# Performance work log

Measured on AMD Instinct MI355X. Metric: run time of the kernel, lower is better.

Reference implementation:

```python
import jax, jax.numpy as jnp
import numpy as np
import math

D_MODEL, D_HEAD = 1024, 64
N_HEADS = D_MODEL // D_HEAD  # 16
EPS = 1e-6

def rms_norm(x, scale, eps=EPS):
    ms = jnp.mean(x * x, axis=-1, keepdims=True)
    return x * scale * jax.lax.rsqrt(ms + eps)

def apply_rotary_emb(x, theta):
    # theta: (..., d) rotates first 2*d dims of x
    d = theta.shape[-1]
    x1, x2, x3 = x[..., :d], x[..., d:2 * d], x[..., 2 * d:]
    cos, sin = jnp.cos(theta), jnp.sin(theta)
    return jnp.concatenate([x1 * cos - x2 * sin, x2 * cos + x1 * sin, x3], axis=-1)

def make_freqs():
    d4 = D_HEAD // 4  # 16
    log_min, log_max = math.log(math.pi), math.log(10.0 * math.pi)
    f = np.exp(np.linspace(log_min, log_max, N_HEADS * d4 + 1, dtype=np.float64)[:-1])
    return jnp.asarray(f.reshape(d4, N_HEADS).T, dtype=jnp.float32)  # (n_heads, d_head//4)

def setup_inputs() -> dict:
    key = jax.random.key(0)
    ks = jax.random.split(key, 8)
    n, l = 4, 1024
    x = jax.random.normal(ks[0], (n, l, D_MODEL), jnp.float32)
    pos = jax.random.uniform(ks[1], (n, l, 2), jnp.float32)
    attn_mask = jnp.ones((1, 1, l, l), dtype=bool)
    cond = jax.random.normal(ks[2], (n, 1, D_MODEL), jnp.float32)
    norm_w = jax.random.normal(ks[3], (D_MODEL, D_MODEL), jnp.float32) * 0.02
    qkv_w = jax.random.normal(ks[4], (3 * D_MODEL, D_MODEL), jnp.float32) * (D_MODEL ** -0.5)
    qk_scale = jnp.ones((N_HEADS, 1, 1), jnp.float32)
    out_w = jax.random.normal(ks[5], (D_MODEL, D_MODEL), jnp.float32) * 0.02
    freqs = make_freqs()
    return {"x": x, "pos": pos, "attn_mask": attn_mask, "cond": cond,
            "norm_w": norm_w, "qkv_w": qkv_w, "qk_scale": qk_scale,
            "freqs": freqs, "out_w": out_w}

def reference(x, pos, attn_mask, cond, norm_w, qkv_w, qk_scale, freqs, out_w):
    n, l, d = x.shape
    # AdaRMSNorm
    h = rms_norm(x, jnp.einsum('nlc,dc->nld', cond, norm_w) + 1.0)
    # QKV projection -> (n, h, l, e)
    qkv = jnp.einsum('nld,ed->nle', h, qkv_w)
    q, k, v = jnp.split(qkv, 3, axis=-1)
    split_heads = lambda t: t.reshape(n, l, N_HEADS, D_HEAD).transpose(0, 2, 1, 3)
    q, k, v = split_heads(q), split_heads(k), split_heads(v)
    # per-head RMSNorm (scale shape (h,1,1))
    q = rms_norm(q, qk_scale)
    k = rms_norm(k, qk_scale)
    # axial RoPE: theta (n, h, l, d_head//2)
    theta = jnp.concatenate([
        pos[:, None, :, 0:1] * freqs[None, :, None, :],
        pos[:, None, :, 1:2] * freqs[None, :, None, :],
    ], axis=-1)
    q = apply_rotary_emb(q, theta)
    k = apply_rotary_emb(k, theta)
    # SDPA
    scores = jnp.einsum('nhqe,nhke->nhqk', q, k) * (D_HEAD ** -0.5)
    scores = jnp.where(attn_mask, scores, jnp.float32(-1e30))
    attn = jax.nn.softmax(scores, axis=-1)
    o = jnp.einsum('nhqk,nhke->nhqe', attn, v)
    o = o.transpose(0, 2, 1, 3).reshape(n, l, d)
    return jnp.einsum('nld,ed->nle', o, out_w)
```

## Files before the change

### kernel.cpp

```cpp
#include <hip/hip_runtime.h>

typedef short bf16x8 __attribute__((ext_vector_type(8)));
typedef float f32x4 __attribute__((ext_vector_type(4)));

__device__ __forceinline__ float bf2f(ushort u) {
  union { unsigned int i; float f; } x; x.i = ((unsigned int)u) << 16; return x.f;
}
__device__ __forceinline__ ushort f2bf(float f) {
  union { float f; unsigned int i; } x; x.f = f;
  unsigned int r = x.i + 0x7fff + ((x.i >> 16) & 1);
  return (ushort)(r >> 16);
}
__device__ __forceinline__ unsigned int cvtpk_bf16(float a, float b) {
  unsigned int r;
  asm("v_cvt_pk_bf16_f32 %0, %1, %2" : "=v"(r) : "v"(a), "v"(b));
  return r;
}

__device__ __forceinline__ f32x4 mfma16(bf16x8 a, bf16x8 b, f32x4 c) {
  return __builtin_amdgcn_mfma_f32_16x16x32_bf16(a, b, c, 0, 0, 0);
}

__device__ __forceinline__ void gload_lds16(const void* g, void* l) {
  __builtin_amdgcn_global_load_lds(
      (const __attribute__((address_space(1))) void*)g,
      (__attribute__((address_space(3))) void*)l, 16, 0, 0);
}

__global__ __launch_bounds__(256) void f2bf_vec2(const float* __restrict__ a,
                                                 ushort* __restrict__ oa, int n4a,
                                                 const float* __restrict__ b,
                                                 ushort* __restrict__ ob, int n4b) {
  int i = blockIdx.x * 256 + threadIdx.x;
  const float* src;
  ushort* dst;
  int j;
  if (i < n4a) {
    src = a; dst = oa; j = i;
  } else {
    j = i - n4a;
    if (j >= n4b) return;
    src = b; dst = ob;
  }
  float4 v = ((const float4*)src)[j];
  ushort4 o;
  o.x = f2bf(v.x); o.y = f2bf(v.y); o.z = f2bf(v.z); o.w = f2bf(v.w);
  ((ushort4*)dst)[j] = o;
}

__global__ __launch_bounds__(256) void cond_gemv(const float* __restrict__ cond,
                                                 const float* __restrict__ nw,
                                                 float* __restrict__ sout) {
  const int w = threadIdx.x >> 6, lane = threadIdx.x & 63;
  const int idx = blockIdx.x * 4 + w;
  const int n_ = idx >> 10, d = idx & 1023;
  const float* cr = cond + n_ * 1024;
  const float* wr_ = nw + (size_t)d * 1024;
  float sum = 0.f;
#pragma unroll
  for (int c = lane; c < 1024; c += 64) sum += cr[c] * wr_[c];
#pragma unroll
  for (int off = 1; off < 64; off <<= 1) sum += __shfl_xor(sum, off);
  if (lane == 0) sout[idx] = sum + 1.0f;
}

__global__ __launch_bounds__(256) void rmsnorm_x(const float* __restrict__ x,
                                                 const float* __restrict__ s,
                                                 ushort* __restrict__ h, int L) {
  const int row = blockIdx.x;
  const int n_ = row / L;
  const int tid = threadIdx.x;
  __shared__ float red[4];
  float4 xv = ((const float4*)(x + (size_t)row * 1024))[tid];
  float ss = xv.x * xv.x + xv.y * xv.y + xv.z * xv.z + xv.w * xv.w;
#pragma unroll
  for (int off = 1; off < 64; off <<= 1) ss += __shfl_xor(ss, off);
  if ((tid & 63) == 0) red[tid >> 6] = ss;
  __syncthreads();
  float tot = red[0] + red[1] + red[2] + red[3];
  float r = rsqrtf(tot * (1.f / 1024.f) + 1e-6f);
  float4 sv = ((const float4*)(s + (size_t)n_ * 1024))[tid];
  ushort4 o;
  o.x = f2bf(xv.x * sv.x * r);
  o.y = f2bf(xv.y * sv.y * r);
  o.z = f2bf(xv.z * sv.z * r);
  o.w = f2bf(xv.w * sv.w * r);
  ((ushort4*)(h + (size_t)row * 1024))[tid] = o;
}

template <typename OT>
__global__ __launch_bounds__(256) void gemm_bt(const ushort* __restrict__ A,
                                               const ushort* __restrict__ B,
                                               OT* __restrict__ C, int M, int N,
                                               int K, int nbx) {
  __shared__ ushort As[2][128 * 32];
  __shared__ ushort Bs[2][128 * 32];
  const int tid = threadIdx.x;
  const int w = tid >> 6;
  const int lane = tid & 63;
  const int wr = w >> 1, wc = w & 1;
  const int lm = lane & 15, g = lane >> 4;
  const int qchunk = gridDim.x >> 3;
  const int swz = (blockIdx.x & 7) * qchunk + (blockIdx.x >> 3);
  const int bn = (swz % nbx) * 128;
  const int bm = (swz / nbx) * 128;
  f32x4 acc[4][4] = {};
  const int u_ = lane >> 3;
  const int pp = (lane & 7) ^ u_;
  const int srow = (u_ << 1) | (pp >> 2);
  const int scol = (pp & 3) * 8;
  const int rb = (lm >> 1) * 64 + (((((lm & 1) << 2) | g) ^ (lm >> 1)) << 3);

  auto stage = [&](int kt, int b) {
#pragma unroll
    for (int i = 0; i < 2; ++i) {
      const int c = w * 2 + i;
      gload_lds16(&A[(size_t)(bm + c * 16 + srow) * K + kt + scol],
                  &As[b][c * 512]);
      gload_lds16(&B[(size_t)(bn + c * 16 + srow) * K + kt + scol],
                  &Bs[b][c * 512]);
    }
  };

  const int NTK = K >> 5;
  stage(0, 0);
  stage(32, 1);
  for (int t = 0; t < NTK; ++t) {
    const int b = t & 1;
    if (t + 1 < NTK)
      asm volatile("s_waitcnt vmcnt(4)" ::: "memory");
    else
      asm volatile("s_waitcnt vmcnt(0)" ::: "memory");
    __builtin_amdgcn_s_barrier();
    bf16x8 af[4], bfr[4];
#pragma unroll
    for (int mi = 0; mi < 4; ++mi)
      af[mi] = *(const bf16x8*)&As[b][(wr * 4 + mi) * 512 + rb];
#pragma unroll
    for (int ni = 0; ni < 4; ++ni)
      bfr[ni] = *(const bf16x8*)&Bs[b][(wc * 4 + ni) * 512 + rb];
    asm volatile("s_waitcnt lgkmcnt(0)" ::: "memory");
    __builtin_amdgcn_sched_barrier(0);
    __builtin_amdgcn_s_barrier();
    if (t + 2 < NTK) stage((t + 2) << 5, b);
#pragma unroll
    for (int mi = 0; mi < 4; ++mi)
#pragma unroll
      for (int ni = 0; ni < 4; ++ni)
        acc[mi][ni] = mfma16(af[mi], bfr[ni], acc[mi][ni]);
  }
#pragma unroll
  for (int mi = 0; mi < 4; ++mi)
#pragma unroll
    for (int ni = 0; ni < 4; ++ni) {
      int col = bn + wc * 64 + ni * 16 + lm;
#pragma unroll
      for (int r = 0; r < 4; ++r) {
        int row = bm + wr * 64 + mi * 16 + g * 4 + r;
        float v = acc[mi][ni][r];
        if constexpr (sizeof(OT) == 2)
          C[(size_t)row * N + col] = (OT)f2bf(v);
        else
          C[(size_t)row * N + col] = (OT)v;
      }
    }
}

__global__ __launch_bounds__(256) void qkv_prep(
    const ushort* __restrict__ qkv, const float* __restrict__ pos,
    const float* __restrict__ qscale, const float* __restrict__ freqs,
    ushort* __restrict__ Qr, ushort* __restrict__ Kr, ushort* __restrict__ Vr,
    int L) {
  const int row = blockIdx.x;
  const int n_ = row / L;
  const int l = row - n_ * L;
  const int w = threadIdx.x >> 6, lane = threadIdx.x & 63;
  const float p0 = pos[row * 2 + 0], p1 = pos[row * 2 + 1];
  const int tl = lane & 31;
#pragma unroll
  for (int hi = 0; hi < 4; ++hi) {
    const int h = w * 4 + hi;
    const size_t ib = (size_t)row * 3072 + h * 64 + lane;
    float qv = bf2f(qkv[ib]);
    float kv = bf2f(qkv[ib + 1024]);
    float vv = bf2f(qkv[ib + 2048]);
    float sq = qv * qv, sk = kv * kv;
#pragma unroll
    for (int off = 1; off < 64; off <<= 1) {
      sq += __shfl_xor(sq, off);
      sk += __shfl_xor(sk, off);
    }
    const float sc = qscale[h];
    float qn = qv * sc * rsqrtf(sq * (1.f / 64.f) + 1e-6f);
    float kn = kv * sc * rsqrtf(sk * (1.f / 64.f) + 1e-6f);
    float th = ((tl < 16) ? p0 : p1) * freqs[h * 16 + (tl & 15)];
    float s_, c_;
    sincosf(th, &s_, &c_);
    float qo = __shfl_xor(qn, 32);
    float ko = __shfl_xor(kn, 32);
    float qr = (lane < 32) ? (qn * c_ - qo * s_) : (qn * c_ + qo * s_);
    float kr = (lane < 32) ? (kn * c_ - ko * s_) : (kn * c_ + ko * s_);
    const size_t ob = ((size_t)(n_ * 16 + h) * L + l) * 64 + lane;
    Qr[ob] = f2bf(qr * 0.18033688f);
    Kr[ob] = f2bf(kr);
    Vr[ob] = f2bf(vv);
  }
}

__global__ __launch_bounds__(256) void vtrans(const ushort* __restrict__ v,
                                              ushort* __restrict__ vt) {
  __shared__ ushort T[64][72];
  const int tid = threadIdx.x;
  const int nh = blockIdx.y;
  const int l0 = blockIdx.x * 64;
  const int lr = tid >> 2;
  const int d0 = (tid & 3) * 16;
  const ushort* src = v + ((size_t)nh * 1024 + l0 + lr) * 64 + d0;
  *(uint4*)&T[lr][d0] = *(const uint4*)src;
  *(uint4*)&T[lr][d0 + 8] = *(const uint4*)(src + 8);
  __syncthreads();
  const int d = tid >> 2;
  const int lc = (tid & 3) * 16;
  ushort tmp[16];
#pragma unroll
  for (int j = 0; j < 16; ++j) tmp[j] = T[lc + j][d];
  ushort* dst = vt + ((size_t)nh * 64 + d) * 1024 + l0 + lc;
  *(uint4*)dst = *(uint4*)&tmp[0];
  *(uint4*)(dst + 8) = *(uint4*)&tmp[8];
}

__global__ __launch_bounds__(256) void attn_kernel(
    const ushort* __restrict__ Q, const ushort* __restrict__ Kg,
    const ushort* __restrict__ Vtg, ushort* __restrict__ O, int L) {
  __shared__ ushort Ks[2][64 * 64];
  __shared__ ushort Vs[2][64 * 64];
  __shared__ ushort Pb[4][32 * 64];
  const int tid = threadIdx.x;
  const int w = tid >> 6, lane = tid & 63;
  const int lm = lane & 15, g = lane >> 4;
  const int swz = (blockIdx.x & 7) * 64 + (blockIdx.x >> 3);
  const int nh = swz >> 3;
  const int qt = swz & 7;
  const ushort* q = Q + (size_t)nh * L * 64;
  const ushort* k = Kg + (size_t)nh * L * 64;
  const ushort* vt = Vtg + (size_t)nh * 64 * L;
  const int qbase = qt * 128 + w * 32;
  bf16x8 qf[2][2];
#pragma unroll
  for (int qs = 0; qs < 2; ++qs)
#pragma unroll
    for (int kc = 0; kc < 2; ++kc)
      qf[qs][kc] = *(const bf16x8*)&q[(size_t)(qbase + qs * 16 + lm) * 64 +
                                      kc * 32 + g * 8];
  f32x4 ot[2][4] = {};
  f32x4 lsacc[2] = {};
  bf16x8 ones;
#pragma unroll
  for (int i = 0; i < 8; ++i) ones[i] = (short)0x3F80;
  const int sr = lane >> 3;
  const int ss = (lane & 7) ^ sr;

  auto stage = [&](int tt, int b) {
#pragma unroll
    for (int i = 0; i < 2; ++i) {
      const int r = w * 16 + i * 8 + sr;
      gload_lds16(&k[(size_t)(tt * 64 + r) * 64 + ss * 8],
                  &Ks[b][(w * 16 + i * 8) * 64]);
    }
#pragma unroll
    for (int i = 0; i < 2; ++i) {
      const int r = w * 16 + i * 8 + sr;
      gload_lds16(&vt[(size_t)r * L + tt * 64 + ss * 8],
                  &Vs[b][(w * 16 + i * 8) * 64]);
    }
  };

  stage(0, 0);
  __syncthreads();
  const int NT = L >> 6;
  for (int t = 0; t < NT; ++t) {
    const int cur = t & 1;
    if (t + 1 < NT) stage(t + 1, cur ^ 1);
    const ushort* ksb = &Ks[cur][0];
    f32x4 st[2][4] = {};
    __builtin_amdgcn_s_setprio(1);
#pragma unroll
    for (int t16 = 0; t16 < 4; ++t16) {
      const int r = t16 * 16 + lm;
#pragma unroll
      for (int kc = 0; kc < 2; ++kc) {
        bf16x8 a = *(const bf16x8*)&ksb[r * 64 + (((kc * 4 + g) ^ (lm & 7)) << 3)];
        st[0][t16] = mfma16(a, qf[0][kc], st[0][t16]);
        st[1][t16] = mfma16(a, qf[1][kc], st[1][t16]);
      }
    }
    __builtin_amdgcn_s_setprio(0);
    float e[2][4][4];
#pragma unroll
    for (int qs = 0; qs < 2; ++qs)
#pragma unroll
      for (int t16 = 0; t16 < 4; ++t16)
#pragma unroll
        for (int r = 0; r < 4; ++r)
          e[qs][t16][r] = __builtin_amdgcn_exp2f(st[qs][t16][r]);
    ushort* pb = &Pb[w][0];
#pragma unroll
    for (int qs = 0; qs < 2; ++qs)
#pragma unroll
      for (int t16 = 0; t16 < 4; ++t16) {
        unsigned int lo = cvtpk_bf16(e[qs][t16][0], e[qs][t16][1]);
        unsigned int hi = cvtpk_bf16(e[qs][t16][2], e[qs][t16][3]);
        const int slot = (t16 * 2 + (g >> 1)) ^ (lm & 7);
        *(uint2*)&pb[(qs * 16 + lm) * 64 + slot * 8 + (g & 1) * 4] =
            make_uint2(lo, hi);
      }
    asm volatile("s_waitcnt lgkmcnt(0)" ::: "memory");
    __builtin_amdgcn_sched_barrier(0);
    bf16x8 pf[2][2];
#pragma unroll
    for (int qs = 0; qs < 2; ++qs)
#pragma unroll
      for (int c = 0; c < 2; ++c)
        pf[qs][c] = *(const bf16x8*)&pb[(qs * 16 + lm) * 64 +
                                        (((c * 4 + g) ^ (lm & 7)) << 3)];
    const ushort* vsb = &Vs[cur][0];
    __builtin_amdgcn_s_setprio(1);
#pragma unroll
    for (int db = 0; db < 4; ++db) {
      const int d = db * 16 + lm;
#pragma unroll
      for (int c = 0; c < 2; ++c) {
        bf16x8 a = *(const bf16x8*)&vsb[d * 64 + (((c * 4 + g) ^ (lm & 7)) << 3)];
        ot[0][db] = mfma16(a, pf[0][c], ot[0][db]);
        ot[1][db] = mfma16(a, pf[1][c], ot[1][db]);
      }
    }
#pragma unroll
    for (int qs = 0; qs < 2; ++qs)
#pragma unroll
      for (int c = 0; c < 2; ++c)
        lsacc[qs] = mfma16(ones, pf[qs][c], lsacc[qs]);
    __builtin_amdgcn_s_setprio(0);
    __syncthreads();
  }
  const int n_ = nh >> 4, h = nh & 15;
#pragma unroll
  for (int qs = 0; qs < 2; ++qs) {
    const float inv = 1.f / lsacc[qs][0];
#pragma unroll
    for (int db = 0; db < 4; ++db) {
      unsigned int lo = cvtpk_bf16(ot[qs][db][0] * inv, ot[qs][db][1] * inv);
      unsigned int hi = cvtpk_bf16(ot[qs][db][2] * inv, ot[qs][db][3] * inv);
      size_t off = ((size_t)(n_ * L + qbase + qs * 16 + lm) * 1024) + h * 64 +
                   db * 16 + g * 4;
      *(uint2*)&O[off] = make_uint2(lo, hi);
    }
  }
}

extern "C" void kernel_launch(void* const* d_in, const int* in_sizes, int n_in,
                              void* d_out, int out_size, void* d_ws,
                              size_t ws_size, hipStream_t stream) {
  const float* x = (const float*)d_in[0];
  const float* pos = (const float*)d_in[1];
  const float* cond = (const float*)d_in[3];
  const float* norm_w = (const float*)d_in[4];
  const float* qkv_w = (const float*)d_in[5];
  const float* qk_scale = (const float*)d_in[6];
  const float* freqs = (const float*)d_in[7];
  const float* out_w = (const float*)d_in[8];
  float* out = (float*)d_out;
  const int L = 1024;

  char* wsb = (char*)d_ws;
  ushort* qkvw_bf = (ushort*)(wsb);
  ushort* outw_bf = (ushort*)(wsb + 6291456);
  float* s_cond = (float*)(wsb + 8388608);
  ushort* h_buf = (ushort*)(wsb + 8404992);
  ushort* qkv_buf = (ushort*)(wsb + 16793600);
  ushort* q_r = (ushort*)(wsb + 41959424);
  ushort* k_r = (ushort*)(wsb + 50348032);
  ushort* v_r = (ushort*)(wsb + 58736640);
  ushort* o_buf = (ushort*)(wsb + 67125248);
  ushort* vt_buf = h_buf;

  hipLaunchKernelGGL(f2bf_vec2, dim3(4096), dim3(256), 0, stream, qkv_w,
                     qkvw_bf, 786432, out_w, outw_bf, 262144);
  hipLaunchKernelGGL(cond_gemv, dim3(1024), dim3(256), 0, stream, cond, norm_w,
                     s_cond);
  hipLaunchKernelGGL(rmsnorm_x, dim3(4096), dim3(256), 0, stream, x, s_cond,
                     h_buf, L);
  hipLaunchKernelGGL(gemm_bt<ushort>, dim3(768), dim3(256), 0, stream, h_buf,
                     qkvw_bf, qkv_buf, 4096, 3072, 1024, 24);
  hipLaunchKernelGGL(qkv_prep, dim3(4096), dim3(256), 0, stream, qkv_buf, pos,
                     qk_scale, freqs, q_r, k_r, v_r, L);
  hipLaunchKernelGGL(vtrans, dim3(16, 64), dim3(256), 0, stream, v_r, vt_buf);
  hipLaunchKernelGGL(attn_kernel, dim3(512), dim3(256), 0, stream, q_r, k_r,
                     vt_buf, o_buf, L);
  hipLaunchKernelGGL(gemm_bt<float>, dim3(256), dim3(256), 0, stream, o_buf,
                     outw_bf, out, 4096, 1024, 1024, 8);
}
```

Baseline: 120.9 us.

## Switch attention to 32x32x16 MFMA and keep P in registers via permlane swap

```diff
diff --git a/kernel.cpp b/kernel.cpp
--- a/kernel.cpp
+++ b/kernel.cpp
@@ -2,6 +2,7 @@
 
 typedef short bf16x8 __attribute__((ext_vector_type(8)));
 typedef float f32x4 __attribute__((ext_vector_type(4)));
+typedef float f32x16 __attribute__((ext_vector_type(16)));
 
 __device__ __forceinline__ float bf2f(ushort u) {
   union { unsigned int i; float f; } x; x.i = ((unsigned int)u) << 16; return x.f;
@@ -19,6 +20,12 @@
 
 __device__ __forceinline__ f32x4 mfma16(bf16x8 a, bf16x8 b, f32x4 c) {
   return __builtin_amdgcn_mfma_f32_16x16x32_bf16(a, b, c, 0, 0, 0);
+}
+__device__ __forceinline__ f32x16 mfma32(bf16x8 a, bf16x8 b, f32x16 c) {
+  return __builtin_amdgcn_mfma_f32_32x32x16_bf16(a, b, c, 0, 0, 0);
+}
+__device__ __forceinline__ void plswap(unsigned int& a, unsigned int& b) {
+  asm volatile("v_permlane32_swap_b32 %0, %1" : "+v"(a), "+v"(b));
 }
 
 __device__ __forceinline__ void gload_lds16(const void* g, void* l) {
@@ -234,10 +241,9 @@
     const ushort* __restrict__ Vtg, ushort* __restrict__ O, int L) {
   __shared__ ushort Ks[2][64 * 64];
   __shared__ ushort Vs[2][64 * 64];
-  __shared__ ushort Pb[4][32 * 64];
   const int tid = threadIdx.x;
   const int w = tid >> 6, lane = tid & 63;
-  const int lm = lane & 15, g = lane >> 4;
+  const int l31 = lane & 31, h32 = lane >> 5;
   const int swz = (blockIdx.x & 7) * 64 + (blockIdx.x >> 3);
   const int nh = swz >> 3;
   const int qt = swz & 7;
@@ -245,15 +251,11 @@
   const ushort* k = Kg + (size_t)nh * L * 64;
   const ushort* vt = Vtg + (size_t)nh * 64 * L;
   const int qbase = qt * 128 + w * 32;
-  bf16x8 qf[2][2];
-#pragma unroll
-  for (int qs = 0; qs < 2; ++qs)
-#pragma unroll
-    for (int kc = 0; kc < 2; ++kc)
-      qf[qs][kc] = *(const bf16x8*)&q[(size_t)(qbase + qs * 16 + lm) * 64 +
-                                      kc * 32 + g * 8];
-  f32x4 ot[2][4] = {};
-  f32x4 lsacc[2] = {};
+  bf16x8 qf[4];
+#pragma unroll
+  for (int kt = 0; kt < 4; ++kt)
+    qf[kt] = *(const bf16x8*)&q[(size_t)(qbase + l31) * 64 + kt * 16 + h32 * 8];
+  f32x16 ot0 = {}, ot1 = {}, lsacc = {};
   bf16x8 ones;
 #pragma unroll
   for (int i = 0; i < 8; ++i) ones[i] = (short)0x3F80;
@@ -282,78 +284,63 @@
     const int cur = t & 1;
     if (t + 1 < NT) stage(t + 1, cur ^ 1);
     const ushort* ksb = &Ks[cur][0];
-    f32x4 st[2][4] = {};
+    f32x16 st0 = {}, st1 = {};
     __builtin_amdgcn_s_setprio(1);
 #pragma unroll
-    for (int t16 = 0; t16 < 4; ++t16) {
-      const int r = t16 * 16 + lm;
-#pragma unroll
-      for (int kc = 0; kc < 2; ++kc) {
-        bf16x8 a = *(const bf16x8*)&ksb[r * 64 + (((kc * 4 + g) ^ (lm & 7)) << 3)];
-        st[0][t16] = mfma16(a, qf[0][kc], st[0][t16]);
-        st[1][t16] = mfma16(a, qf[1][kc], st[1][t16]);
-      }
+    for (int kk = 0; kk < 4; ++kk) {
+      const int sl = (((kk * 2 + h32) ^ (l31 & 7)) << 3);
+      bf16x8 a0 = *(const bf16x8*)&ksb[l31 * 64 + sl];
+      bf16x8 a1 = *(const bf16x8*)&ksb[(32 + l31) * 64 + sl];
+      st0 = mfma32(a0, qf[kk], st0);
+      st1 = mfma32(a1, qf[kk], st1);
     }
     __builtin_amdgcn_s_setprio(0);
-    float e[2][4][4];
-#pragma unroll
-    for (int qs = 0; qs < 2; ++qs)
-#pragma unroll
-      for (int t16 = 0; t16 < 4; ++t16)
-#pragma unroll
-        for (int r = 0; r < 4; ++r)
-          e[qs][t16][r] = __builtin_amdgcn_exp2f(st[qs][t16][r]);
-    ushort* pb = &Pb[w][0];
-#pragma unroll
-    for (int qs = 0; qs < 2; ++qs)
-#pragma unroll
-      for (int t16 = 0; t16 < 4; ++t16) {
-        unsigned int lo = cvtpk_bf16(e[qs][t16][0], e[qs][t16][1]);
-        unsigned int hi = cvtpk_bf16(e[qs][t16][2], e[qs][t16][3]);
-        const int slot = (t16 * 2 + (g >> 1)) ^ (lm & 7);
-        *(uint2*)&pb[(qs * 16 + lm) * 64 + slot * 8 + (g & 1) * 4] =
-            make_uint2(lo, hi);
-      }
-    asm volatile("s_waitcnt lgkmcnt(0)" ::: "memory");
-    __builtin_amdgcn_sched_barrier(0);
-    bf16x8 pf[2][2];
-#pragma unroll
-    for (int qs = 0; qs < 2; ++qs)
-#pragma unroll
-      for (int c = 0; c < 2; ++c)
-        pf[qs][c] = *(const bf16x8*)&pb[(qs * 16 + lm) * 64 +
-                                        (((c * 4 + g) ^ (lm & 7)) << 3)];
+    bf16x8 pfm[4];
+#pragma unroll
+    for (int kt2 = 0; kt2 < 2; ++kt2) {
+      float e[16];
+#pragma unroll
+      for (int r = 0; r < 16; ++r)
+        e[r] = __builtin_amdgcn_exp2f(kt2 ? st1[r] : st0[r]);
+      unsigned int A0 = cvtpk_bf16(e[0], e[1]), A1 = cvtpk_bf16(e[2], e[3]);
+      unsigned int B0 = cvtpk_bf16(e[4], e[5]), B1 = cvtpk_bf16(e[6], e[7]);
+      unsigned int C0 = cvtpk_bf16(e[8], e[9]), C1 = cvtpk_bf16(e[10], e[11]);
+      unsigned int D0 = cvtpk_bf16(e[12], e[13]), D1 = cvtpk_bf16(e[14], e[15]);
+      plswap(A0, B0);
+      plswap(A1, B1);
+      plswap(C0, D0);
+      plswap(C1, D1);
+      union { unsigned int u[4]; bf16x8 v; } f0, f1;
+      f0.u[0] = A0; f0.u[1] = A1; f0.u[2] = B0; f0.u[3] = B1;
+      f1.u[0] = C0; f1.u[1] = C1; f1.u[2] = D0; f1.u[3] = D1;
+      pfm[kt2 * 2 + 0] = f0.v;
+      pfm[kt2 * 2 + 1] = f1.v;
+    }
     const ushort* vsb = &Vs[cur][0];
     __builtin_amdgcn_s_setprio(1);
 #pragma unroll
-    for (int db = 0; db < 4; ++db) {
-      const int d = db * 16 + lm;
-#pragma unroll
-      for (int c = 0; c < 2; ++c) {
-        bf16x8 a = *(const bf16x8*)&vsb[d * 64 + (((c * 4 + g) ^ (lm & 7)) << 3)];
-        ot[0][db] = mfma16(a, pf[0][c], ot[0][db]);
-        ot[1][db] = mfma16(a, pf[1][c], ot[1][db]);
-      }
-    }
-#pragma unroll
-    for (int qs = 0; qs < 2; ++qs)
-#pragma unroll
-      for (int c = 0; c < 2; ++c)
-        lsacc[qs] = mfma16(ones, pf[qs][c], lsacc[qs]);
+    for (int m = 0; m < 4; ++m) {
+      const int sl = (((m * 2 + h32) ^ (l31 & 7)) << 3);
+      bf16x8 a0 = *(const bf16x8*)&vsb[l31 * 64 + sl];
+      bf16x8 a1 = *(const bf16x8*)&vsb[(32 + l31) * 64 + sl];
+      ot0 = mfma32(a0, pfm[m], ot0);
+      ot1 = mfma32(a1, pfm[m], ot1);
+      lsacc = mfma32(ones, pfm[m], lsacc);
+    }
     __builtin_amdgcn_s_setprio(0);
     __syncthreads();
   }
+  const float inv = 1.f / lsacc[0];
   const int n_ = nh >> 4, h = nh & 15;
-#pragma unroll
-  for (int qs = 0; qs < 2; ++qs) {
-    const float inv = 1.f / lsacc[qs][0];
-#pragma unroll
-    for (int db = 0; db < 4; ++db) {
-      unsigned int lo = cvtpk_bf16(ot[qs][db][0] * inv, ot[qs][db][1] * inv);
-      unsigned int hi = cvtpk_bf16(ot[qs][db][2] * inv, ot[qs][db][3] * inv);
-      size_t off = ((size_t)(n_ * L + qbase + qs * 16 + lm) * 1024) + h * 64 +
-                   db * 16 + g * 4;
-      *(uint2*)&O[off] = make_uint2(lo, hi);
+  const size_t rowoff = ((size_t)(n_ * L + qbase + l31)) * 1024 + h * 64;
+#pragma unroll
+  for (int dt = 0; dt < 2; ++dt) {
+    const f32x16& o = dt ? ot1 : ot0;
+#pragma unroll
+    for (int qd = 0; qd < 4; ++qd) {
+      unsigned int w0 = cvtpk_bf16(o[qd * 4 + 0] * inv, o[qd * 4 + 1] * inv);
+      unsigned int w1 = cvtpk_bf16(o[qd * 4 + 2] * inv, o[qd * 4 + 3] * inv);
+      *(uint2*)&O[rowoff + dt * 32 + qd * 8 + h32 * 4] = make_uint2(w0, w1);
     }
   }
 }
```

Measured after the change: 124.8 us. 3.2% more time.

## Fuse weight cast with cond GEMV, and V transpose into QKV prep

Applied to the files above, without the earlier changes.

```diff
diff --git a/kernel.cpp b/kernel.cpp
--- a/kernel.cpp
+++ b/kernel.cpp
@@ -27,32 +27,29 @@
       (__attribute__((address_space(3))) void*)l, 16, 0, 0);
 }
 
-__global__ __launch_bounds__(256) void f2bf_vec2(const float* __restrict__ a,
-                                                 ushort* __restrict__ oa, int n4a,
-                                                 const float* __restrict__ b,
-                                                 ushort* __restrict__ ob, int n4b) {
-  int i = blockIdx.x * 256 + threadIdx.x;
-  const float* src;
-  ushort* dst;
-  int j;
-  if (i < n4a) {
-    src = a; dst = oa; j = i;
-  } else {
-    j = i - n4a;
-    if (j >= n4b) return;
-    src = b; dst = ob;
-  }
-  float4 v = ((const float4*)src)[j];
-  ushort4 o;
-  o.x = f2bf(v.x); o.y = f2bf(v.y); o.z = f2bf(v.z); o.w = f2bf(v.w);
-  ((ushort4*)dst)[j] = o;
-}
-
-__global__ __launch_bounds__(256) void cond_gemv(const float* __restrict__ cond,
-                                                 const float* __restrict__ nw,
-                                                 float* __restrict__ sout) {
+__global__ __launch_bounds__(256) void prep0(
+    const float* __restrict__ qkv_w, ushort* __restrict__ qkvw_bf,
+    const float* __restrict__ out_w, ushort* __restrict__ outw_bf,
+    const float* __restrict__ cond, const float* __restrict__ nw,
+    float* __restrict__ sout) {
+  const int b = blockIdx.x;
+  if (b < 4096) {
+    const float* src;
+    ushort* dst;
+    int j;
+    if (b < 3072) {
+      src = qkv_w; dst = qkvw_bf; j = b * 256 + threadIdx.x;
+    } else {
+      src = out_w; dst = outw_bf; j = (b - 3072) * 256 + threadIdx.x;
+    }
+    float4 v = ((const float4*)src)[j];
+    ushort4 o;
+    o.x = f2bf(v.x); o.y = f2bf(v.y); o.z = f2bf(v.z); o.w = f2bf(v.w);
+    ((ushort4*)dst)[j] = o;
+    return;
+  }
   const int w = threadIdx.x >> 6, lane = threadIdx.x & 63;
-  const int idx = blockIdx.x * 4 + w;
+  const int idx = (b - 4096) * 4 + w;
   const int n_ = idx >> 10, d = idx & 1023;
   const float* cr = cond + n_ * 1024;
   const float* wr_ = nw + (size_t)d * 1024;
@@ -166,20 +163,26 @@
     }
 }
 
-__global__ __launch_bounds__(256) void qkv_prep(
+__global__ __launch_bounds__(256) void qkv_prep_t(
     const ushort* __restrict__ qkv, const float* __restrict__ pos,
     const float* __restrict__ qscale, const float* __restrict__ freqs,
-    ushort* __restrict__ Qr, ushort* __restrict__ Kr, ushort* __restrict__ Vr,
+    ushort* __restrict__ Qr, ushort* __restrict__ Kr, ushort* __restrict__ Vt,
     int L) {
-  const int row = blockIdx.x;
-  const int n_ = row / L;
-  const int l = row - n_ * L;
-  const int w = threadIdx.x >> 6, lane = threadIdx.x & 63;
-  const float p0 = pos[row * 2 + 0], p1 = pos[row * 2 + 1];
+  __shared__ ushort T[64][72];
+  const int tid = threadIdx.x;
+  const int w = tid >> 6, lane = tid & 63;
+  const int bid = blockIdx.x;
+  const int nh = bid >> 4;
+  const int lc = bid & 15;
+  const int n_ = nh >> 4, h = nh & 15;
+  const int l0 = lc * 64;
+  const float sc = qscale[h];
   const int tl = lane & 31;
-#pragma unroll
-  for (int hi = 0; hi < 4; ++hi) {
-    const int h = w * 4 + hi;
+  const float fr = freqs[h * 16 + (tl & 15)];
+#pragma unroll
+  for (int i = 0; i < 16; ++i) {
+    const int r = i * 4 + w;
+    const int row = n_ * L + l0 + r;
     const size_t ib = (size_t)row * 3072 + h * 64 + lane;
     float qv = bf2f(qkv[ib]);
     float kv = bf2f(qkv[ib + 1024]);
@@ -190,41 +193,28 @@
       sq += __shfl_xor(sq, off);
       sk += __shfl_xor(sk, off);
     }
-    const float sc = qscale[h];
     float qn = qv * sc * rsqrtf(sq * (1.f / 64.f) + 1e-6f);
     float kn = kv * sc * rsqrtf(sk * (1.f / 64.f) + 1e-6f);
-    float th = ((tl < 16) ? p0 : p1) * freqs[h * 16 + (tl & 15)];
+    const float p0 = pos[row * 2 + 0], p1 = pos[row * 2 + 1];
+    float th = ((tl < 16) ? p0 : p1) * fr;
     float s_, c_;
     sincosf(th, &s_, &c_);
     float qo = __shfl_xor(qn, 32);
     float ko = __shfl_xor(kn, 32);
     float qr = (lane < 32) ? (qn * c_ - qo * s_) : (qn * c_ + qo * s_);
     float kr = (lane < 32) ? (kn * c_ - ko * s_) : (kn * c_ + ko * s_);
-    const size_t ob = ((size_t)(n_ * 16 + h) * L + l) * 64 + lane;
+    const size_t ob = ((size_t)nh * L + l0 + r) * 64 + lane;
     Qr[ob] = f2bf(qr * 0.18033688f);
     Kr[ob] = f2bf(kr);
-    Vr[ob] = f2bf(vv);
-  }
-}
-
-__global__ __launch_bounds__(256) void vtrans(const ushort* __restrict__ v,
-                                              ushort* __restrict__ vt) {
-  __shared__ ushort T[64][72];
-  const int tid = threadIdx.x;
-  const int nh = blockIdx.y;
-  const int l0 = blockIdx.x * 64;
-  const int lr = tid >> 2;
-  const int d0 = (tid & 3) * 16;
-  const ushort* src = v + ((size_t)nh * 1024 + l0 + lr) * 64 + d0;
-  *(uint4*)&T[lr][d0] = *(const uint4*)src;
-  *(uint4*)&T[lr][d0 + 8] = *(const uint4*)(src + 8);
+    T[r][lane] = f2bf(vv);
+  }
   __syncthreads();
   const int d = tid >> 2;
-  const int lc = (tid & 3) * 16;
+  const int lc4 = (tid & 3) * 16;
   ushort tmp[16];
 #pragma unroll
-  for (int j = 0; j < 16; ++j) tmp[j] = T[lc + j][d];
-  ushort* dst = vt + ((size_t)nh * 64 + d) * 1024 + l0 + lc;
+  for (int j = 0; j < 16; ++j) tmp[j] = T[lc4 + j][d];
+  ushort* dst = Vt + ((size_t)nh * 64 + d) * L + l0 + lc4;
   *(uint4*)dst = *(uint4*)&tmp[0];
   *(uint4*)(dst + 8) = *(uint4*)&tmp[8];
 }
@@ -380,21 +370,17 @@
   ushort* qkv_buf = (ushort*)(wsb + 16793600);
   ushort* q_r = (ushort*)(wsb + 41959424);
   ushort* k_r = (ushort*)(wsb + 50348032);
-  ushort* v_r = (ushort*)(wsb + 58736640);
   ushort* o_buf = (ushort*)(wsb + 67125248);
   ushort* vt_buf = h_buf;
 
-  hipLaunchKernelGGL(f2bf_vec2, dim3(4096), dim3(256), 0, stream, qkv_w,
-                     qkvw_bf, 786432, out_w, outw_bf, 262144);
-  hipLaunchKernelGGL(cond_gemv, dim3(1024), dim3(256), 0, stream, cond, norm_w,
-                     s_cond);
+  hipLaunchKernelGGL(prep0, dim3(5120), dim3(256), 0, stream, qkv_w, qkvw_bf,
+                     out_w, outw_bf, cond, norm_w, s_cond);
   hipLaunchKernelGGL(rmsnorm_x, dim3(4096), dim3(256), 0, stream, x, s_cond,
                      h_buf, L);
   hipLaunchKernelGGL(gemm_bt<ushort>, dim3(768), dim3(256), 0, stream, h_buf,
                      qkvw_bf, qkv_buf, 4096, 3072, 1024, 24);
-  hipLaunchKernelGGL(qkv_prep, dim3(4096), dim3(256), 0, stream, qkv_buf, pos,
-                     qk_scale, freqs, q_r, k_r, v_r, L);
-  hipLaunchKernelGGL(vtrans, dim3(16, 64), dim3(256), 0, stream, v_r, vt_buf);
+  hipLaunchKernelGGL(qkv_prep_t, dim3(1024), dim3(256), 0, stream, qkv_buf,
+                     pos, qk_scale, freqs, q_r, k_r, vt_buf, L);
   hipLaunchKernelGGL(attn_kernel, dim3(512), dim3(256), 0, stream, q_r, k_r,
                      vt_buf, o_buf, L);
   hipLaunchKernelGGL(gemm_bt<float>, dim3(256), dim3(256), 0, stream, o_buf,
```

Measured after the change: 116.9 us. -3.3%, faster.
